# Kernel tuning notes

Measured on AMD Instinct MI355X. Metric: run time of the kernel, lower is better.

The kernel has to match this reference:

```python
import jax, jax.numpy as jnp
import numpy as np

N_DRUGS, N_TARGETS, N_ENT = 2000, 4000, 6000
NUM_RELS, REL_DIM, FEAT = 8, 64, 512
N_TRI = 131072
IN1 = 2 * FEAT + REL_DIM  # 1088


def setup_inputs() -> dict:
    key = jax.random.key(0)
    ks = jax.random.split(key, 12)
    # id2rel pattern: utype = drug iff r % 2 == 0; vtype = drug iff (r // 2) % 2 == 0
    rels = np.arange(NUM_RELS)
    u_is_drug = jnp.asarray(rels % 2 == 0)
    v_is_drug = jnp.asarray((rels // 2) % 2 == 0)
    triplets = jnp.stack([
        jax.random.randint(ks[0], (N_TRI,), 0, N_ENT, dtype=jnp.int32),
        jax.random.randint(ks[1], (N_TRI,), 0, N_ENT, dtype=jnp.int32),
        jax.random.randint(ks[2], (N_TRI,), 0, NUM_RELS, dtype=jnp.int32),
    ], axis=1)
    return {
        "d_intra": jax.random.normal(ks[3], (N_DRUGS, FEAT), jnp.float32),
        "d_inter": jax.random.normal(ks[4], (N_DRUGS, FEAT), jnp.float32),
        "t_intra": jax.random.normal(ks[5], (N_TARGETS, FEAT), jnp.float32),
        "t_inter": jax.random.normal(ks[6], (N_TARGETS, FEAT), jnp.float32),
        "did_sub": jax.random.randint(ks[7], (N_ENT,), 0, N_DRUGS, dtype=jnp.int32),
        "tid_sub": jax.random.randint(ks[8], (N_ENT,), 0, N_TARGETS, dtype=jnp.int32),
        "triplets": triplets,
        "u_is_drug": u_is_drug,
        "v_is_drug": v_is_drug,
        "rel_emb_intra": jax.random.normal(ks[9], (NUM_RELS, REL_DIM), jnp.float32) * 0.1,
        "rel_emb_inter": jax.random.normal(ks[10], (NUM_RELS, REL_DIM), jnp.float32) * 0.1,
        "W_intra": jax.random.normal(ks[11], (IN1, 1), jnp.float32) * 0.03,
        "b_intra": jnp.zeros((1,), jnp.float32),
        "W_inter": jax.random.normal(jax.random.fold_in(key, 99), (IN1, 1), jnp.float32) * 0.03,
        "b_inter": jnp.zeros((1,), jnp.float32),
    }


def _branch_logits(d_feat, t_feat, rel_emb, W, b, did, tid, u, v, r, u_drug, v_drug):
    # Conditional gather: drug-table row if type is 'drug', else target-table row.
    fu = jnp.where(u_drug[:, None], d_feat[did[u]], t_feat[tid[u]])  # [N, FEAT]
    fv = jnp.where(v_drug[:, None], d_feat[did[v]], t_feat[tid[v]])  # [N, FEAT]
    re = rel_emb[r]                                                  # [N, REL_DIM]
    # Equivalent to concat([fu, fv, re]) @ W + b, done blockwise (no big concat).
    Wu, Wv, Wr = W[:FEAT], W[FEAT:2 * FEAT], W[2 * FEAT:]
    return fu @ Wu + fv @ Wv + re @ Wr + b  # [N, 1]


def reference(d_intra, d_inter, t_intra, t_inter, did_sub, tid_sub, triplets,
              u_is_drug, v_is_drug, rel_emb_intra, rel_emb_inter,
              W_intra, b_intra, W_inter, b_inter):
    a1, a2 = 0.6, 0.2
    u, v, r = triplets[:, 0], triplets[:, 1], triplets[:, 2]
    ud, vd = u_is_drug[r], v_is_drug[r]  # per-triplet type flags via id2rel[r]
    s1 = _branch_logits(d_intra, t_intra, rel_emb_intra, W_intra, b_intra,
                        did_sub, tid_sub, u, v, r, ud, vd)
    s2 = _branch_logits(d_inter, t_inter, rel_emb_inter, W_inter, b_inter,
                        did_sub, tid_sub, u, v, r, ud, vd)
    return a1 * jnp.tanh(s1) + a2 * jnp.tanh(s2)
```

## Files before the change

### kernel.cpp

```cpp
#include <hip/hip_runtime.h>

#define FEAT 512
#define REL_DIM 64
#define N_DRUGS 2000
#define N_TARGETS 4000
#define N_ENT_ROWS (N_DRUGS + N_TARGETS)
#define N_TRI 131072

__device__ __forceinline__ float dot4(float4 a, float4 b) {
    return a.x * b.x + a.y * b.y + a.z * b.z + a.w * b.w;
}

__device__ __forceinline__ float waveReduce(float v) {
#pragma unroll
    for (int off = 32; off; off >>= 1) v += __shfl_xor(v, off, 64);
    return v;
}

__device__ __forceinline__ float fast_tanh(float x) {
    const float e = __expf(2.0f * x);
    return 1.0f - 2.0f * __builtin_amdgcn_rcpf(e + 1.0f);
}

__global__ __launch_bounds__(256) void precompute_kernel(
    const float* __restrict__ d_intra, const float* __restrict__ d_inter,
    const float* __restrict__ t_intra, const float* __restrict__ t_inter,
    const float* __restrict__ rel_emb_intra, const float* __restrict__ rel_emb_inter,
    const float* __restrict__ W_intra, const float* __restrict__ b_intra,
    const float* __restrict__ W_inter, const float* __restrict__ b_inter,
    float2* __restrict__ preU, float2* __restrict__ preV,
    float2* __restrict__ relC)
{
    const int wave = threadIdx.x >> 6;
    const int lane = threadIdx.x & 63;
    const int row  = blockIdx.x * 4 + wave;

    if (row < N_ENT_ROWS) {
        const float* fA;
        const float* fB;
        if (row < N_DRUGS) {
            fA = d_intra + (size_t)row * FEAT;
            fB = d_inter + (size_t)row * FEAT;
        } else {
            const int t = row - N_DRUGS;
            fA = t_intra + (size_t)t * FEAT;
            fB = t_inter + (size_t)t * FEAT;
        }
        const float4* a4 = (const float4*)fA;
        const float4* b4 = (const float4*)fB;
        const float4* w1 = (const float4*)W_intra;
        const float4* w2 = (const float4*)W_inter;

        const float4 aA0 = a4[lane],        aA1 = a4[lane + 64];
        const float4 bB0 = b4[lane],        bB1 = b4[lane + 64];
        const float4 wu10 = w1[lane],       wu11 = w1[lane + 64];
        const float4 wv10 = w1[lane + 128], wv11 = w1[lane + 192];
        const float4 wu20 = w2[lane],       wu21 = w2[lane + 64];
        const float4 wv20 = w2[lane + 128], wv21 = w2[lane + 192];

        float s_u1 = dot4(aA0, wu10) + dot4(aA1, wu11);
        float s_v1 = dot4(aA0, wv10) + dot4(aA1, wv11);
        float s_u2 = dot4(bB0, wu20) + dot4(bB1, wu21);
        float s_v2 = dot4(bB0, wv20) + dot4(bB1, wv21);

        s_u1 = waveReduce(s_u1);
        s_v1 = waveReduce(s_v1);
        s_u2 = waveReduce(s_u2);
        s_v2 = waveReduce(s_v2);

        if (lane == 0) {
            preU[row] = make_float2(s_u1, s_u2);
            preV[row] = make_float2(s_v1, s_v2);
        }
    } else if (row == N_ENT_ROWS) {
        const float b1 = b_intra[0];
        const float b2 = b_inter[0];
        const float wr1 = W_intra[2 * FEAT + lane];
        const float wr2 = W_inter[2 * FEAT + lane];
#pragma unroll
        for (int r = 0; r < 8; ++r) {
            float p1 = rel_emb_intra[r * REL_DIM + lane] * wr1;
            float p2 = rel_emb_inter[r * REL_DIM + lane] * wr2;
            p1 = waveReduce(p1);
            p2 = waveReduce(p2);
            if (lane == 0) relC[r] = make_float2(p1 + b1, p2 + b2);
        }
    }
}

__global__ __launch_bounds__(256) void triplet_kernel(
    const int2* __restrict__ tri2,
    const int* __restrict__ did_sub, const int* __restrict__ tid_sub,
    const float2* __restrict__ preU, const float2* __restrict__ preV,
    const float2* __restrict__ relC,
    float2* __restrict__ out2)
{
    const int i = blockIdx.x * blockDim.x + threadIdx.x;
    const int2 p0 = tri2[3 * i + 0];
    const int2 p1 = tri2[3 * i + 1];
    const int2 p2 = tri2[3 * i + 2];

    const int us[2] = {p0.x, p1.y};
    const int vs[2] = {p0.y, p2.x};
    const int rs[2] = {p1.x, p2.y};
    float res[2];

#pragma unroll
    for (int k = 0; k < 2; ++k) {
        const int u = us[k], v = vs[k], r = rs[k];
        const bool ud = (r & 1) == 0;
        const bool vd = ((r >> 1) & 1) == 0;
        const int du = did_sub[u], tu = tid_sub[u];
        const int dv = did_sub[v], tv = tid_sub[v];
        const int iu = ud ? du : tu + N_DRUGS;
        const int iv = vd ? dv : tv + N_DRUGS;
        const float2 cu = preU[iu];
        const float2 cv = preV[iv];
        const float2 cr = relC[r];
        const float s1 = cu.x + cv.x + cr.x;
        const float s2 = cu.y + cv.y + cr.y;
        res[k] = 0.6f * fast_tanh(s1) + 0.2f * fast_tanh(s2);
    }
    out2[i] = make_float2(res[0], res[1]);
}

extern "C" void kernel_launch(void* const* d_in, const int* in_sizes, int n_in,
                              void* d_out, int out_size, void* d_ws, size_t ws_size,
                              hipStream_t stream) {
    const float* d_intra        = (const float*)d_in[0];
    const float* d_inter        = (const float*)d_in[1];
    const float* t_intra        = (const float*)d_in[2];
    const float* t_inter        = (const float*)d_in[3];
    const int*   did_sub        = (const int*)d_in[4];
    const int*   tid_sub        = (const int*)d_in[5];
    const int*   triplets       = (const int*)d_in[6];
    const float* rel_emb_intra  = (const float*)d_in[9];
    const float* rel_emb_inter  = (const float*)d_in[10];
    const float* W_intra        = (const float*)d_in[11];
    const float* b_intra        = (const float*)d_in[12];
    const float* W_inter        = (const float*)d_in[13];
    const float* b_inter        = (const float*)d_in[14];

    float2* ws   = (float2*)d_ws;
    float2* preU = ws;
    float2* preV = ws + N_ENT_ROWS;
    float2* relC = preV + N_ENT_ROWS;

    const int rows  = N_ENT_ROWS + 1;
    const int gridA = (rows + 3) / 4;
    precompute_kernel<<<gridA, 256, 0, stream>>>(
        d_intra, d_inter, t_intra, t_inter,
        rel_emb_intra, rel_emb_inter,
        W_intra, b_intra, W_inter, b_inter,
        preU, preV, relC);

    const int gridB = (N_TRI / 2 + 255) / 256;
    triplet_kernel<<<gridB, 256, 0, stream>>>(
        (const int2*)triplets, did_sub, tid_sub, preU, preV, relC, (float2*)d_out);
}
```

Before: 101.9 us.

## Fuse precompute and triplet kernels with grid-wide atomic barrier

Merges the two launches into one persistent kernel of 256 blocks of 1024 threads. Each thread first loads its triplet and the index lookups, then waves compute the per-entity projections, all blocks meet at an atomic-counter barrier, and each thread finishes its triplet. This removes a kernel launch boundary and overlaps the index-gather latency with the projection work. It adds a memset launch, relies on all 256 blocks being resident at once (otherwise the barrier deadlocks), and drops the two-triplets-per-thread vectorized output.

```diff
diff --git a/kernel.cpp b/kernel.cpp
--- a/kernel.cpp
+++ b/kernel.cpp
@@ -6,6 +6,9 @@
 #define N_TARGETS 4000
 #define N_ENT_ROWS (N_DRUGS + N_TARGETS)
 #define N_TRI 131072
+#define NBLOCKS 256
+#define NTHREADS 1024
+#define TOTAL_WAVES (NBLOCKS * NTHREADS / 64)
 
 __device__ __forceinline__ float dot4(float4 a, float4 b) {
     return a.x * b.x + a.y * b.y + a.z * b.z + a.w * b.w;
@@ -22,106 +25,109 @@
     return 1.0f - 2.0f * __builtin_amdgcn_rcpf(e + 1.0f);
 }
 
-__global__ __launch_bounds__(256) void precompute_kernel(
+__global__ __launch_bounds__(NTHREADS) void fused_kernel(
     const float* __restrict__ d_intra, const float* __restrict__ d_inter,
     const float* __restrict__ t_intra, const float* __restrict__ t_inter,
     const float* __restrict__ rel_emb_intra, const float* __restrict__ rel_emb_inter,
     const float* __restrict__ W_intra, const float* __restrict__ b_intra,
     const float* __restrict__ W_inter, const float* __restrict__ b_inter,
+    const int* __restrict__ triplets,
+    const int* __restrict__ did_sub, const int* __restrict__ tid_sub,
     float2* __restrict__ preU, float2* __restrict__ preV,
-    float2* __restrict__ relC)
+    float2* __restrict__ relC, unsigned* __restrict__ ctr,
+    float* __restrict__ out)
 {
-    const int wave = threadIdx.x >> 6;
-    const int lane = threadIdx.x & 63;
-    const int row  = blockIdx.x * 4 + wave;
+    const int tid   = threadIdx.x;
+    const int wave  = tid >> 6;
+    const int lane  = tid & 63;
+    const int gwave = blockIdx.x * (NTHREADS / 64) + wave;
+    const int gtid  = blockIdx.x * NTHREADS + tid;
 
-    if (row < N_ENT_ROWS) {
-        const float* fA;
-        const float* fB;
-        if (row < N_DRUGS) {
-            fA = d_intra + (size_t)row * FEAT;
-            fB = d_inter + (size_t)row * FEAT;
+    int t_u = 0, t_v = 0, t_r = 0, iu = 0, iv = 0;
+    const bool do_tri = gtid < N_TRI;
+    if (do_tri) {
+        t_u = triplets[3 * gtid + 0];
+        t_v = triplets[3 * gtid + 1];
+        t_r = triplets[3 * gtid + 2];
+        const bool ud = (t_r & 1) == 0;
+        const bool vd = ((t_r >> 1) & 1) == 0;
+        iu = ud ? did_sub[t_u] : tid_sub[t_u] + N_DRUGS;
+        iv = vd ? did_sub[t_v] : tid_sub[t_v] + N_DRUGS;
+    }
+
+    for (int row = gwave; row < N_ENT_ROWS + 1; row += TOTAL_WAVES) {
+        if (row < N_ENT_ROWS) {
+            const float* fA;
+            const float* fB;
+            if (row < N_DRUGS) {
+                fA = d_intra + (size_t)row * FEAT;
+                fB = d_inter + (size_t)row * FEAT;
+            } else {
+                const int t = row - N_DRUGS;
+                fA = t_intra + (size_t)t * FEAT;
+                fB = t_inter + (size_t)t * FEAT;
+            }
+            const float4* a4 = (const float4*)fA;
+            const float4* b4 = (const float4*)fB;
+            const float4* w1 = (const float4*)W_intra;
+            const float4* w2 = (const float4*)W_inter;
+
+            const float4 aA0 = a4[lane],        aA1 = a4[lane + 64];
+            const float4 bB0 = b4[lane],        bB1 = b4[lane + 64];
+            const float4 wu10 = w1[lane],       wu11 = w1[lane + 64];
+            const float4 wv10 = w1[lane + 128], wv11 = w1[lane + 192];
+            const float4 wu20 = w2[lane],       wu21 = w2[lane + 64];
+            const float4 wv20 = w2[lane + 128], wv21 = w2[lane + 192];
+
+            float s_u1 = dot4(aA0, wu10) + dot4(aA1, wu11);
+            float s_v1 = dot4(aA0, wv10) + dot4(aA1, wv11);
+            float s_u2 = dot4(bB0, wu20) + dot4(bB1, wu21);
+            float s_v2 = dot4(bB0, wv20) + dot4(bB1, wv21);
+
+            s_u1 = waveReduce(s_u1);
+            s_v1 = waveReduce(s_v1);
+            s_u2 = waveReduce(s_u2);
+            s_v2 = waveReduce(s_v2);
+
+            if (lane == 0) {
+                preU[row] = make_float2(s_u1, s_u2);
+                preV[row] = make_float2(s_v1, s_v2);
+            }
         } else {
-            const int t = row - N_DRUGS;
-            fA = t_intra + (size_t)t * FEAT;
-            fB = t_inter + (size_t)t * FEAT;
-        }
-        const float4* a4 = (const float4*)fA;
-        const float4* b4 = (const float4*)fB;
-        const float4* w1 = (const float4*)W_intra;
-        const float4* w2 = (const float4*)W_inter;
-
-        const float4 aA0 = a4[lane],        aA1 = a4[lane + 64];
-        const float4 bB0 = b4[lane],        bB1 = b4[lane + 64];
-        const float4 wu10 = w1[lane],       wu11 = w1[lane + 64];
-        const float4 wv10 = w1[lane + 128], wv11 = w1[lane + 192];
-        const float4 wu20 = w2[lane],       wu21 = w2[lane + 64];
-        const float4 wv20 = w2[lane + 128], wv21 = w2[lane + 192];
-
-        float s_u1 = dot4(aA0, wu10) + dot4(aA1, wu11);
-        float s_v1 = dot4(aA0, wv10) + dot4(aA1, wv11);
-        float s_u2 = dot4(bB0, wu20) + dot4(bB1, wu21);
-        float s_v2 = dot4(bB0, wv20) + dot4(bB1, wv21);
-
-        s_u1 = waveReduce(s_u1);
-        s_v1 = waveReduce(s_v1);
-        s_u2 = waveReduce(s_u2);
-        s_v2 = waveReduce(s_v2);
-
-        if (lane == 0) {
-            preU[row] = make_float2(s_u1, s_u2);
-            preV[row] = make_float2(s_v1, s_v2);
-        }
-    } else if (row == N_ENT_ROWS) {
-        const float b1 = b_intra[0];
-        const float b2 = b_inter[0];
-        const float wr1 = W_intra[2 * FEAT + lane];
-        const float wr2 = W_inter[2 * FEAT + lane];
+            const float b1 = b_intra[0];
+            const float b2 = b_inter[0];
+            const float wr1 = W_intra[2 * FEAT + lane];
+            const float wr2 = W_inter[2 * FEAT + lane];
 #pragma unroll
-        for (int r = 0; r < 8; ++r) {
-            float p1 = rel_emb_intra[r * REL_DIM + lane] * wr1;
-            float p2 = rel_emb_inter[r * REL_DIM + lane] * wr2;
-            p1 = waveReduce(p1);
-            p2 = waveReduce(p2);
-            if (lane == 0) relC[r] = make_float2(p1 + b1, p2 + b2);
+            for (int r = 0; r < 8; ++r) {
+                float p1 = rel_emb_intra[r * REL_DIM + lane] * wr1;
+                float p2 = rel_emb_inter[r * REL_DIM + lane] * wr2;
+                p1 = waveReduce(p1);
+                p2 = waveReduce(p2);
+                if (lane == 0) relC[r] = make_float2(p1 + b1, p2 + b2);
+            }
         }
     }
-}
 
-__global__ __launch_bounds__(256) void triplet_kernel(
-    const int2* __restrict__ tri2,
-    const int* __restrict__ did_sub, const int* __restrict__ tid_sub,
-    const float2* __restrict__ preU, const float2* __restrict__ preV,
-    const float2* __restrict__ relC,
-    float2* __restrict__ out2)
-{
-    const int i = blockIdx.x * blockDim.x + threadIdx.x;
-    const int2 p0 = tri2[3 * i + 0];
-    const int2 p1 = tri2[3 * i + 1];
-    const int2 p2 = tri2[3 * i + 2];
+    __threadfence();
+    __syncthreads();
+    if (tid == 0) {
+        __hip_atomic_fetch_add(ctr, 1u, __ATOMIC_ACQ_REL, __HIP_MEMORY_SCOPE_AGENT);
+        while (__hip_atomic_load(ctr, __ATOMIC_ACQUIRE, __HIP_MEMORY_SCOPE_AGENT)
+               < (unsigned)NBLOCKS) {
+            __builtin_amdgcn_s_sleep(8);
+        }
+    }
+    __syncthreads();
 
-    const int us[2] = {p0.x, p1.y};
-    const int vs[2] = {p0.y, p2.x};
-    const int rs[2] = {p1.x, p2.y};
-    float res[2];
-
-#pragma unroll
-    for (int k = 0; k < 2; ++k) {
-        const int u = us[k], v = vs[k], r = rs[k];
-        const bool ud = (r & 1) == 0;
-        const bool vd = ((r >> 1) & 1) == 0;
-        const int du = did_sub[u], tu = tid_sub[u];
-        const int dv = did_sub[v], tv = tid_sub[v];
-        const int iu = ud ? du : tu + N_DRUGS;
-        const int iv = vd ? dv : tv + N_DRUGS;
+    if (do_tri) {
         const float2 cu = preU[iu];
         const float2 cv = preV[iv];
-        const float2 cr = relC[r];
+        const float2 cr = relC[t_r];
         const float s1 = cu.x + cv.x + cr.x;
         const float s2 = cu.y + cv.y + cr.y;
-        res[k] = 0.6f * fast_tanh(s1) + 0.2f * fast_tanh(s2);
+        out[gtid] = 0.6f * fast_tanh(s1) + 0.2f * fast_tanh(s2);
     }
-    out2[i] = make_float2(res[0], res[1]);
 }
 
 extern "C" void kernel_launch(void* const* d_in, const int* in_sizes, int n_in,
@@ -141,20 +147,18 @@
     const float* W_inter        = (const float*)d_in[13];
     const float* b_inter        = (const float*)d_in[14];
 
-    float2* ws   = (float2*)d_ws;
-    float2* preU = ws;
-    float2* preV = ws + N_ENT_ROWS;
-    float2* relC = preV + N_ENT_ROWS;
+    float2* ws    = (float2*)d_ws;
+    float2* preU  = ws;
+    float2* preV  = ws + N_ENT_ROWS;
+    float2* relC  = preV + N_ENT_ROWS;
+    unsigned* ctr = (unsigned*)(relC + 8);
 
-    const int rows  = N_ENT_ROWS + 1;
-    const int gridA = (rows + 3) / 4;
-    precompute_kernel<<<gridA, 256, 0, stream>>>(
+    hipMemsetAsync(ctr, 0, sizeof(unsigned), stream);
+
+    fused_kernel<<<NBLOCKS, NTHREADS, 0, stream>>>(
         d_intra, d_inter, t_intra, t_inter,
         rel_emb_intra, rel_emb_inter,
         W_intra, b_intra, W_inter, b_inter,
-        preU, preV, relC);
-
-    const int gridB = (N_TRI / 2 + 255) / 256;
-    triplet_kernel<<<gridB, 256, 0, stream>>>(
-        (const int2*)triplets, did_sub, tid_sub, preU, preV, relC, (float2*)d_out);
+        triplets, did_sub, tid_sub,
+        preU, preV, relC, ctr, (float*)d_out);
 }
```

Measured after the change: 219.0 us. 115% more time.
